# Performance work log

Hardware: AMD Instinct MI355X
Metric: run time of the kernel (lower is better)

## Reference

```python
import jax, jax.numpy as jnp
import numpy as np

HIDDEN = 768
NUM_HEADS = 12
HEAD_DIM = HIDDEN // NUM_HEADS
NUM_SELECTED = 64
SCALE = 1.0 / np.sqrt(HEAD_DIM)


def setup_inputs() -> dict:
    key = jax.random.key(0)
    k0, k1, k2, k3, k4 = jax.random.split(key, 5)
    B, S = 1, 2048
    inputs = jax.random.normal(k0, (B, S, HIDDEN), dtype=jnp.float32)
    # nn.Linear weights, stored as [out, in]; applied as x @ W.T
    Wq = jax.random.normal(k1, (HIDDEN, HIDDEN), dtype=jnp.float32) * 0.02
    Wk = jax.random.normal(k2, (HIDDEN, HIDDEN), dtype=jnp.float32) * 0.02
    Wv = jax.random.normal(k3, (HIDDEN, HIDDEN), dtype=jnp.float32) * 0.02
    Wo = jax.random.normal(k4, (HIDDEN, HIDDEN), dtype=jnp.float32) * 0.02
    return {"inputs": inputs, "Wq": Wq, "Wk": Wk, "Wv": Wv, "Wo": Wo}


def reference(inputs, Wq, Wk, Wv, Wo):
    B, S, H = inputs.shape
    K = NUM_SELECTED
    pos = jnp.arange(S)
    window_starts = jnp.clip(pos + 1 - K, 0, None)                      # [S]
    sel = window_starts[:, None] + jnp.arange(K)[None, :]               # [S, K]
    sel = jnp.clip(sel, 0, S - 1)
    causal_mask = sel <= pos[:, None]                                   # [S, K]

    # Per-token linear projections; gathering after the (per-token) linear is
    # mathematically identical to the original gather-then-project.
    q = inputs @ Wq.T                                                   # [B,S,H]
    k_full = inputs @ Wk.T                                              # [B,S,H]
    v_full = inputs @ Wv.T                                              # [B,S,H]

    k = k_full[:, sel]                                                  # [B,S,K,H]
    v = v_full[:, sel]                                                  # [B,S,K,H]

    q = q.reshape(B, S, NUM_HEADS, HEAD_DIM)                            # [B,S,n,d]
    k = k.reshape(B, S, K, NUM_HEADS, HEAD_DIM)                         # [B,S,K,n,d]
    v = v.reshape(B, S, K, NUM_HEADS, HEAD_DIM)

    scores = jnp.einsum("bsnd,bsknd->bnsk", q, k) * SCALE               # [B,n,S,K]
    scores = jnp.where(causal_mask[None, None], scores, -jnp.inf)
    weights = jax.nn.softmax(scores, axis=-1)                           # [B,n,S,K]

    out = jnp.einsum("bnsk,bsknd->bsnd", weights, v)                    # [B,S,n,d]
    out = out.reshape(B, S, H)
    return out @ Wo.T
```

## Files before the change

### kernel.cpp

```cpp
#include <hip/hip_runtime.h>
#include <stdint.h>

#define S_LEN   2048
#define HIDDEN  768
#define NHEADS  12
#define QKV_LD  2304
#define NW      589824

typedef __attribute__((ext_vector_type(8))) short short8;
typedef __attribute__((ext_vector_type(4))) float f32x4;

typedef const __attribute__((address_space(1))) void* gas_ptr;
typedef __attribute__((address_space(3))) void* las_ptr;

__device__ __forceinline__ short f2b(float f) {
    union { float f; uint32_t u; } v; v.f = f;
    uint32_t u = v.u;
    uint32_t r = (u + 0x7FFFu + ((u >> 16) & 1u)) >> 16;
    return (short)r;
}

__global__ __launch_bounds__(256)
void convert_all(const float* __restrict__ X,
                 const float* __restrict__ Wq, const float* __restrict__ Wk,
                 const float* __restrict__ Wv, const float* __restrict__ Wo,
                 short* __restrict__ Xb, short* __restrict__ Wqkvb,
                 short* __restrict__ Wob) {
    const int NX4 = 393216, NW4 = 147456, TOT = 983040;
    for (int idx = blockIdx.x * 256 + threadIdx.x; idx < TOT; idx += 1024 * 256) {
        const float* src; short* dst; int e;
        if (idx < NX4) {
            src = X; dst = Xb; e = idx * 4;
        } else {
            int j = idx - NX4;
            int wb = j / NW4, lb = j % NW4;
            src = wb == 0 ? Wq : wb == 1 ? Wk : wb == 2 ? Wv : Wo;
            dst = wb < 3 ? Wqkvb + wb * NW : Wob;
            e = lb * 4;
        }
        float4 v = *(const float4*)(src + e);
        *(short4*)(dst + e) = make_short4(f2b(v.x), f2b(v.y), f2b(v.z), f2b(v.w));
    }
}

__global__ __launch_bounds__(256)
void gemm_qkv(const short* __restrict__ A, const short* __restrict__ B,
              short* __restrict__ C) {
    __shared__ short sA[3][64 * 64];
    __shared__ short sB[3][128 * 64];

    const int x = blockIdx.x & 7, i = blockIdx.x >> 3;
    const int bm = (x >> 1) * 8 + i / 9;
    const int bn = (x & 1) * 9 + i % 9;

    const int tid = threadIdx.x, lane = tid & 63, w = tid >> 6;
    const int wr = w >> 1, wc = w & 1;

    f32x4 acc[2][4] = {};

    auto stage = [&](int buf, int k0) {
        #pragma unroll
        for (int c = 0; c < 2; ++c) {
            int r = w * 16 + c * 8 + (lane >> 3);
            int scb = ((lane & 7) * 16) ^ ((r & 7) << 4);
            const char* gp = (const char*)(A + (size_t)(bm * 64 + r) * 768 + k0) + scb;
            __builtin_amdgcn_global_load_lds((gas_ptr)gp,
                (las_ptr)((char*)&sA[buf][0] + w * 2048 + c * 1024), 16, 0, 0);
        }
        #pragma unroll
        for (int c = 0; c < 4; ++c) {
            int r = w * 32 + c * 8 + (lane >> 3);
            int scb = ((lane & 7) * 16) ^ ((r & 7) << 4);
            const char* gp = (const char*)(B + (size_t)(bn * 128 + r) * 768 + k0) + scb;
            __builtin_amdgcn_global_load_lds((gas_ptr)gp,
                (las_ptr)((char*)&sB[buf][0] + w * 4096 + c * 1024), 16, 0, 0);
        }
    };

    stage(0, 0);
    stage(1, 64);
    for (int t = 0; t < 12; ++t) {
        if (t < 11) asm volatile("s_waitcnt vmcnt(6)" ::: "memory");
        else        asm volatile("s_waitcnt vmcnt(0)" ::: "memory");
        __builtin_amdgcn_s_barrier();
        asm volatile("" ::: "memory");
        if (t < 10) stage((t + 2) % 3, (t + 2) * 64);

        const char* bA = (const char*)&sA[t % 3][0];
        const char* bB = (const char*)&sB[t % 3][0];
        #pragma unroll
        for (int kh = 0; kh < 2; ++kh) {
            const int kb = kh * 64 + ((lane >> 4) << 4);
            short8 av[2], bv[4];
            #pragma unroll
            for (int mi = 0; mi < 2; ++mi) {
                int row = wr * 32 + mi * 16 + (lane & 15);
                av[mi] = *(const short8*)(bA + row * 128 + (kb ^ ((row & 7) << 4)));
            }
            #pragma unroll
            for (int ni = 0; ni < 4; ++ni) {
                int row = wc * 64 + ni * 16 + (lane & 15);
                bv[ni] = *(const short8*)(bB + row * 128 + (kb ^ ((row & 7) << 4)));
            }
            #pragma unroll
            for (int mi = 0; mi < 2; ++mi)
                #pragma unroll
                for (int ni = 0; ni < 4; ++ni)
                    acc[mi][ni] = __builtin_amdgcn_mfma_f32_16x16x32_bf16(
                        av[mi], bv[ni], acc[mi][ni], 0, 0, 0);
        }
        asm volatile("" ::: "memory");
    }

    const int crow0 = bm * 64 + wr * 32;
    const int ccol0 = bn * 128 + wc * 64;
    #pragma unroll
    for (int mi = 0; mi < 2; ++mi)
        #pragma unroll
        for (int ni = 0; ni < 4; ++ni)
            #pragma unroll
            for (int r = 0; r < 4; ++r) {
                int grow = crow0 + mi * 16 + ((lane >> 4) << 2) + r;
                int gcol = ccol0 + ni * 16 + (lane & 15);
                C[(size_t)grow * QKV_LD + gcol] = f2b(acc[mi][ni][r]);
            }
}

__global__ __launch_bounds__(256)
void gemm_out(const short* __restrict__ A, const short* __restrict__ B,
              float* __restrict__ C) {
    __shared__ short sA[2][64 * 64];
    __shared__ short sB[2][64 * 64];

    const int x = blockIdx.x & 7, i = blockIdx.x >> 3;
    const int bm = (x >> 1) * 8 + i / 6;
    const int bn = (x & 1) * 6 + i % 6;

    const int tid = threadIdx.x, lane = tid & 63, w = tid >> 6;
    const int wr = w >> 1, wc = w & 1;

    f32x4 acc[2][2] = {};

    auto stage = [&](int buf, int k0) {
        #pragma unroll
        for (int c = 0; c < 2; ++c) {
            int r = w * 16 + c * 8 + (lane >> 3);
            int scb = ((lane & 7) * 16) ^ ((r & 7) << 4);
            const char* gpA = (const char*)(A + (size_t)(bm * 64 + r) * 768 + k0) + scb;
            __builtin_amdgcn_global_load_lds((gas_ptr)gpA,
                (las_ptr)((char*)&sA[buf][0] + w * 2048 + c * 1024), 16, 0, 0);
            const char* gpB = (const char*)(B + (size_t)(bn * 64 + r) * 768 + k0) + scb;
            __builtin_amdgcn_global_load_lds((gas_ptr)gpB,
                (las_ptr)((char*)&sB[buf][0] + w * 2048 + c * 1024), 16, 0, 0);
        }
    };

    stage(0, 0);
    __syncthreads();
    int cur = 0;
    for (int t = 0; t < 12; ++t) {
        if (t < 11) stage(cur ^ 1, (t + 1) * 64);
        #pragma unroll
        for (int kh = 0; kh < 2; ++kh) {
            const int kb = kh * 64 + ((lane >> 4) << 4);
            short8 av[2], bv[2];
            #pragma unroll
            for (int mi = 0; mi < 2; ++mi) {
                int row = wr * 32 + mi * 16 + (lane & 15);
                av[mi] = *(const short8*)((const char*)&sA[cur][0] + row * 128 + (kb ^ ((row & 7) << 4)));
            }
            #pragma unroll
            for (int ni = 0; ni < 2; ++ni) {
                int row = wc * 32 + ni * 16 + (lane & 15);
                bv[ni] = *(const short8*)((const char*)&sB[cur][0] + row * 128 + (kb ^ ((row & 7) << 4)));
            }
            #pragma unroll
            for (int mi = 0; mi < 2; ++mi)
                #pragma unroll
                for (int ni = 0; ni < 2; ++ni)
                    acc[mi][ni] = __builtin_amdgcn_mfma_f32_16x16x32_bf16(
                        av[mi], bv[ni], acc[mi][ni], 0, 0, 0);
        }
        __syncthreads();
        cur ^= 1;
    }

    const int crow0 = bm * 64 + wr * 32;
    const int ccol0 = bn * 64 + wc * 32;
    #pragma unroll
    for (int mi = 0; mi < 2; ++mi)
        #pragma unroll
        for (int ni = 0; ni < 2; ++ni)
            #pragma unroll
            for (int r = 0; r < 4; ++r) {
                int grow = crow0 + mi * 16 + ((lane >> 4) << 2) + r;
                int gcol = ccol0 + ni * 16 + (lane & 15);
                C[(size_t)grow * HIDDEN + gcol] = acc[mi][ni][r];
            }
}

__global__ __launch_bounds__(256)
void attn_mfma(const short* __restrict__ QKV, short* __restrict__ O) {
    __shared__ short sK[128 * 64];
    __shared__ short sVt[64 * 128];
    __shared__ short sP[4][16 * 128];

    const int bid = blockIdx.x;
    const int task = (bid & 7) * 48 + (bid >> 3);
    const int h = task % NHEADS;
    const int s0 = (task / NHEADS) * 64;
    const int tid = threadIdx.x, lane = tid & 63, w = tid >> 6;

    #pragma unroll
    for (int c = 0; c < 4; ++c) {
        int r = (w * 4 + c) * 8 + (lane >> 3);
        int gr = s0 - 64 + r; if (gr < 0) gr = 0;
        int scb = ((lane & 7) * 16) ^ ((r & 7) << 4);
        const char* gp = (const char*)(QKV + (size_t)gr * QKV_LD + 768 + h * 64) + scb;
        __builtin_amdgcn_global_load_lds((gas_ptr)gp,
            (las_ptr)((char*)sK + (w * 4 + c) * 1024), 16, 0, 0);
    }
    __builtin_amdgcn_sched_barrier(0);

    const int qrow = w * 16 + (lane & 15);
    short8 qf[2];
    #pragma unroll
    for (int kk = 0; kk < 2; ++kk)
        qf[kk] = *(const short8*)(QKV + (size_t)(s0 + qrow) * QKV_LD + h * 64
                                  + kk * 32 + ((lane >> 4) << 3));
    const int d0 = (tid & 7) * 8;
    const int kbase = (tid >> 3) * 4;
    short8 v[4];
    #pragma unroll
    for (int i = 0; i < 4; ++i) {
        int gr = s0 - 64 + kbase + i; if (gr < 0) gr = 0;
        v[i] = *(const short8*)(QKV + (size_t)gr * QKV_LD + 1536 + h * 64 + d0);
    }

    asm volatile("s_waitcnt vmcnt(6)" ::: "memory");
    __builtin_amdgcn_s_barrier();
    __builtin_amdgcn_sched_barrier(0);

    f32x4 s_acc[8];
    __builtin_amdgcn_s_setprio(1);
    #pragma unroll
    for (int ct = 0; ct < 8; ++ct) {
        s_acc[ct] = (f32x4){0.f, 0.f, 0.f, 0.f};
        int krow = ct * 16 + (lane & 15);
        #pragma unroll
        for (int kk = 0; kk < 2; ++kk) {
            int cb = kk * 64 + ((lane >> 4) << 4);
            short8 kf = *(const short8*)((const char*)sK + krow * 128 + (cb ^ ((krow & 7) << 4)));
            s_acc[ct] = __builtin_amdgcn_mfma_f32_16x16x32_bf16(qf[kk], kf, s_acc[ct], 0, 0, 0);
        }
    }
    __builtin_amdgcn_s_setprio(0);

    const int kcol = lane & 15;
    const int qb = w * 16 + ((lane >> 4) << 2);
    float p[8][4];
    #pragma unroll
    for (int r = 0; r < 4; ++r) {
        int q = qb + r;
        float m = -1e30f;
        #pragma unroll
        for (int ct = 0; ct < 8; ++ct) {
            int kt = ct * 16 + kcol;
            bool valid = (kt > q) && (kt <= q + 64) && (s0 + kt >= 64);
            float sc = valid ? s_acc[ct][r] * 0.125f : -1e30f;
            p[ct][r] = sc;
            m = fmaxf(m, sc);
        }
        #pragma unroll
        for (int off = 1; off < 16; off <<= 1) m = fmaxf(m, __shfl_xor(m, off));
        float sm = 0.f;
        #pragma unroll
        for (int ct = 0; ct < 8; ++ct) {
            float e = __expf(p[ct][r] - m);
            p[ct][r] = e;
            sm += e;
        }
        #pragma unroll
        for (int off = 1; off < 16; off <<= 1) sm += __shfl_xor(sm, off);
        float inv = 1.f / sm;
        #pragma unroll
        for (int ct = 0; ct < 8; ++ct) p[ct][r] *= inv;
    }

    #pragma unroll
    for (int j = 0; j < 8; ++j) {
        int jj = (j + tid) & 7;
        int row = d0 + jj;
        int b = row * 256 + ((kbase * 2) ^ ((row & 7) << 4));
        *(short4*)((char*)sVt + b) = make_short4(v[0][jj], v[1][jj], v[2][jj], v[3][jj]);
    }

    #pragma unroll
    for (int ct = 0; ct < 8; ++ct)
        #pragma unroll
        for (int r = 0; r < 4; ++r) {
            int row = ((lane >> 4) << 2) + r;
            int b = row * 256 + (((ct * 16 + kcol) * 2) ^ ((row & 7) << 4));
            *(short*)((char*)&sP[w][0] + b) = f2b(p[ct][r]);
        }

    __syncthreads();

    short8 pf[4];
    #pragma unroll
    for (int kk = 0; kk < 4; ++kk) {
        int row = lane & 15;
        int cb = kk * 64 + ((lane >> 4) << 4);
        pf[kk] = *(const short8*)((const char*)&sP[w][0] + row * 256 + (cb ^ ((row & 7) << 4)));
    }
    f32x4 o_acc[4];
    __builtin_amdgcn_s_setprio(1);
    #pragma unroll
    for (int nt = 0; nt < 4; ++nt) {
        o_acc[nt] = (f32x4){0.f, 0.f, 0.f, 0.f};
        #pragma unroll
        for (int kk = 0; kk < 4; ++kk) {
            int vrow = nt * 16 + (lane & 15);
            int cb = kk * 64 + ((lane >> 4) << 4);
            short8 vf = *(const short8*)((const char*)sVt + vrow * 256 + (cb ^ ((vrow & 7) << 4)));
            o_acc[nt] = __builtin_amdgcn_mfma_f32_16x16x32_bf16(pf[kk], vf, o_acc[nt], 0, 0, 0);
        }
    }
    __builtin_amdgcn_s_setprio(0);

    #pragma unroll
    for (int nt = 0; nt < 4; ++nt)
        #pragma unroll
        for (int r = 0; r < 4; ++r) {
            int q = s0 + qb + r;
            int dcol = h * 64 + nt * 16 + (lane & 15);
            O[(size_t)q * HIDDEN + dcol] = f2b(o_acc[nt][r]);
        }
}

extern "C" void kernel_launch(void* const* d_in, const int* in_sizes, int n_in,
                              void* d_out, int out_size, void* d_ws, size_t ws_size,
                              hipStream_t stream) {
    const float* X  = (const float*)d_in[0];
    const float* Wq = (const float*)d_in[1];
    const float* Wk = (const float*)d_in[2];
    const float* Wv = (const float*)d_in[3];
    const float* Wo = (const float*)d_in[4];
    float* out = (float*)d_out;

    char* ws = (char*)d_ws;
    short* Xb    = (short*)ws;
    short* Wqkvb = (short*)(ws + 3145728);
    short* Wob   = (short*)(ws + 6684672);
    short* QKVb  = (short*)(ws + 7864320);
    short* Attnb = (short*)(ws + 17301504);

    convert_all<<<1024, 256, 0, stream>>>(X, Wq, Wk, Wv, Wo, Xb, Wqkvb, Wob);
    gemm_qkv<<<576, 256, 0, stream>>>(Xb, Wqkvb, QKVb);
    attn_mfma<<<384, 256, 0, stream>>>(QKVb, Attnb);
    gemm_out<<<384, 256, 0, stream>>>(Attnb, Wob, out);
}
```

Baseline: 50.04 us.

## Enlarge QKV GEMM tile to 128x128 with double buffering; drop setprio in attention

The QKV projection GEMM now uses 128x128 output tiles per block (each wave computes 64x64), which halves the grid to 288 blocks and raises data reuse per LDS load. The three-stage async pipeline with vmcnt waits is replaced by a simpler two-buffer scheme using __syncthreads. The attention kernel also drops its s_setprio hints around the MFMA loops. The trade-off is fewer blocks than the 256 CUs can use well (288 leaves a partial second wave) and a weaker load/compute overlap, in exchange for less global and LDS traffic per FLOP.

```diff
diff --git a/kernel.cpp b/kernel.cpp
--- a/kernel.cpp
+++ b/kernel.cpp
@@ -46,76 +46,69 @@
 __global__ __launch_bounds__(256)
 void gemm_qkv(const short* __restrict__ A, const short* __restrict__ B,
               short* __restrict__ C) {
-    __shared__ short sA[3][64 * 64];
-    __shared__ short sB[3][128 * 64];
+    __shared__ short sA[2][128 * 64];
+    __shared__ short sB[2][128 * 64];
 
     const int x = blockIdx.x & 7, i = blockIdx.x >> 3;
-    const int bm = (x >> 1) * 8 + i / 9;
+    const int bm = (x >> 1) * 4 + i / 9;
     const int bn = (x & 1) * 9 + i % 9;
 
     const int tid = threadIdx.x, lane = tid & 63, w = tid >> 6;
     const int wr = w >> 1, wc = w & 1;
 
-    f32x4 acc[2][4] = {};
+    f32x4 acc[4][4] = {};
+
+    const int st_r_base = w * 32 + (lane >> 3);
+    const int st_cb = (lane & 7) * 16;
 
     auto stage = [&](int buf, int k0) {
         #pragma unroll
-        for (int c = 0; c < 2; ++c) {
-            int r = w * 16 + c * 8 + (lane >> 3);
-            int scb = ((lane & 7) * 16) ^ ((r & 7) << 4);
-            const char* gp = (const char*)(A + (size_t)(bm * 64 + r) * 768 + k0) + scb;
-            __builtin_amdgcn_global_load_lds((gas_ptr)gp,
-                (las_ptr)((char*)&sA[buf][0] + w * 2048 + c * 1024), 16, 0, 0);
-        }
-        #pragma unroll
         for (int c = 0; c < 4; ++c) {
-            int r = w * 32 + c * 8 + (lane >> 3);
-            int scb = ((lane & 7) * 16) ^ ((r & 7) << 4);
-            const char* gp = (const char*)(B + (size_t)(bn * 128 + r) * 768 + k0) + scb;
-            __builtin_amdgcn_global_load_lds((gas_ptr)gp,
+            int r = st_r_base + c * 8;
+            int scb = st_cb ^ ((r & 7) << 4);
+            const char* gpA = (const char*)(A + (size_t)(bm * 128 + r) * 768 + k0) + scb;
+            __builtin_amdgcn_global_load_lds((gas_ptr)gpA,
+                (las_ptr)((char*)&sA[buf][0] + w * 4096 + c * 1024), 16, 0, 0);
+            const char* gpB = (const char*)(B + (size_t)(bn * 128 + r) * 768 + k0) + scb;
+            __builtin_amdgcn_global_load_lds((gas_ptr)gpB,
                 (las_ptr)((char*)&sB[buf][0] + w * 4096 + c * 1024), 16, 0, 0);
         }
     };
 
     stage(0, 0);
-    stage(1, 64);
+    __syncthreads();
+    int cur = 0;
     for (int t = 0; t < 12; ++t) {
-        if (t < 11) asm volatile("s_waitcnt vmcnt(6)" ::: "memory");
-        else        asm volatile("s_waitcnt vmcnt(0)" ::: "memory");
-        __builtin_amdgcn_s_barrier();
-        asm volatile("" ::: "memory");
-        if (t < 10) stage((t + 2) % 3, (t + 2) * 64);
-
-        const char* bA = (const char*)&sA[t % 3][0];
-        const char* bB = (const char*)&sB[t % 3][0];
+        if (t < 11) stage(cur ^ 1, (t + 1) * 64);
         #pragma unroll
         for (int kh = 0; kh < 2; ++kh) {
             const int kb = kh * 64 + ((lane >> 4) << 4);
-            short8 av[2], bv[4];
-            #pragma unroll
-            for (int mi = 0; mi < 2; ++mi) {
-                int row = wr * 32 + mi * 16 + (lane & 15);
-                av[mi] = *(const short8*)(bA + row * 128 + (kb ^ ((row & 7) << 4)));
+            short8 av[4], bv[4];
+            #pragma unroll
+            for (int mi = 0; mi < 4; ++mi) {
+                int row = wr * 64 + mi * 16 + (lane & 15);
+                av[mi] = *(const short8*)((const char*)&sA[cur][0] + row * 128 + (kb ^ ((row & 7) << 4)));
             }
             #pragma unroll
             for (int ni = 0; ni < 4; ++ni) {
                 int row = wc * 64 + ni * 16 + (lane & 15);
-                bv[ni] = *(const short8*)(bB + row * 128 + (kb ^ ((row & 7) << 4)));
-            }
-            #pragma unroll
-            for (int mi = 0; mi < 2; ++mi)
+                bv[ni] = *(const short8*)((const char*)&sB[cur][0] + row * 128 + (kb ^ ((row & 7) << 4)));
+            }
+            #pragma unroll
+            for (int mi = 0; mi < 4; ++mi)
                 #pragma unroll
                 for (int ni = 0; ni < 4; ++ni)
                     acc[mi][ni] = __builtin_amdgcn_mfma_f32_16x16x32_bf16(
                         av[mi], bv[ni], acc[mi][ni], 0, 0, 0);
         }
-        asm volatile("" ::: "memory");
-    }
-
-    const int crow0 = bm * 64 + wr * 32;
+        __syncthreads();
+        cur ^= 1;
+    }
+
+    const int crow0 = bm * 128 + wr * 64;
     const int ccol0 = bn * 128 + wc * 64;
     #pragma unroll
-    for (int mi = 0; mi < 2; ++mi)
+    for (int mi = 0; mi < 4; ++mi)
         #pragma unroll
         for (int ni = 0; ni < 4; ++ni)
             #pragma unroll
@@ -242,7 +235,6 @@
     __builtin_amdgcn_sched_barrier(0);
 
     f32x4 s_acc[8];
-    __builtin_amdgcn_s_setprio(1);
     #pragma unroll
     for (int ct = 0; ct < 8; ++ct) {
         s_acc[ct] = (f32x4){0.f, 0.f, 0.f, 0.f};
@@ -254,7 +246,6 @@
             s_acc[ct] = __builtin_amdgcn_mfma_f32_16x16x32_bf16(qf[kk], kf, s_acc[ct], 0, 0, 0);
         }
     }
-    __builtin_amdgcn_s_setprio(0);
 
     const int kcol = lane & 15;
     const int qb = w * 16 + ((lane >> 4) << 2);
@@ -314,7 +305,6 @@
         pf[kk] = *(const short8*)((const char*)&sP[w][0] + row * 256 + (cb ^ ((row & 7) << 4)));
     }
     f32x4 o_acc[4];
-    __builtin_amdgcn_s_setprio(1);
     #pragma unroll
     for (int nt = 0; nt < 4; ++nt) {
         o_acc[nt] = (f32x4){0.f, 0.f, 0.f, 0.f};
@@ -326,7 +316,6 @@
             o_acc[nt] = __builtin_amdgcn_mfma_f32_16x16x32_bf16(pf[kk], vf, o_acc[nt], 0, 0, 0);
         }
     }
-    __builtin_amdgcn_s_setprio(0);
 
     #pragma unroll
     for (int nt = 0; nt < 4; ++nt)
@@ -356,7 +345,7 @@
     short* Attnb = (short*)(ws + 17301504);
 
     convert_all<<<1024, 256, 0, stream>>>(X, Wq, Wk, Wv, Wo, Xb, Wqkvb, Wob);
-    gemm_qkv<<<576, 256, 0, stream>>>(Xb, Wqkvb, QKVb);
+    gemm_qkv<<<288, 256, 0, stream>>>(Xb, Wqkvb, QKVb);
     attn_mfma<<<384, 256, 0, stream>>>(QKVb, Attnb);
     gemm_out<<<384, 256, 0, stream>>>(Attnb, Wob, out);
 }
```

Result: faster. 45.48 us (-9.1%).
